# Optimization experiments

Hardware: AMD Instinct MI355X
Metric: run time of the kernel (lower is better)

The kernel has to match this reference:

```python
import jax, jax.numpy as jnp
import numpy as np

N_HEADS = 8


def setup_inputs() -> dict:
    key = jax.random.key(0)
    ks = jax.random.split(key, 6)
    B, U, Lx, Ly = 16, 512, 1024, 1024
    x = jax.random.normal(ks[0], (B, U, Lx), dtype=jnp.float32)
    y = jax.random.normal(ks[1], (B, U, Ly), dtype=jnp.float32)
    xy_mask = jax.random.randint(ks[2], (B, Lx, Ly), 0, 2).astype(jnp.bool_)
    wq = jax.random.normal(ks[3], (U, U), dtype=jnp.float32) * (1.0 / np.sqrt(U))
    wk = jax.random.normal(ks[4], (U, U), dtype=jnp.float32) * (1.0 / np.sqrt(U))
    wo = jax.random.normal(ks[5], (U, U), dtype=jnp.float32) * (1.0 / np.sqrt(U))
    return {"x": x, "y": y, "xy_mask": xy_mask, "wq": wq, "wk": wk, "wo": wo}


def reference(x, y, xy_mask, wq, wk, wo):
    # x: (B, U, Lx), y: (B, U, Ly), xy_mask: (B, Lx, Ly)
    B, U, Lx = x.shape
    Ly = y.shape[2]
    H = N_HEADS
    d = U // H
    scale = 1.0 / (d ** 0.5)

    # 1x1 conv (bias=False) == channel-mixing matmul; weight layout (out, in)
    Q = jnp.einsum('ou,bul->bol', wq, x)   # (B, U, Lx)
    K = jnp.einsum('ou,bul->bol', wk, y)   # (B, U, Ly)

    # split channels into heads (head-major channel order, matching torch.split)
    Qh = Q.reshape(B, H, d, Lx)
    Kh = K.reshape(B, H, d, Ly)

    # ReLU-scored attention with mask (no softmax)
    A = jnp.einsum('bhdx,bhdy->bhxy', Qh, Kh)           # (B, H, Lx, Ly)
    A = jnp.maximum(A, 0.0) * scale
    A = jnp.where(xy_mask[:, None, :, :], A, 0.0)

    C = jnp.einsum('bhxy,bhdy->bhdx', A, Kh).reshape(B, U, Lx)

    # per-row element-count normalization (rows with zero count use 1)
    n_el = jnp.maximum(jnp.sum(xy_mask, axis=2), 1)     # (B, Lx)
    C = C / n_el[:, None, :].astype(x.dtype)

    E = 0.5 * (Q + C)
    return jnp.einsum('ou,bul->bol', wo, E)
```

## Files before the change

kernel.cpp:

```cpp
#include <hip/hip_runtime.h>
#include <stdint.h>
#include <stddef.h>

#define B_  16
#define U_  512
#define LX_ 1024
#define LY_ 1024
#define H_  8
#define D_  64

typedef unsigned short ushort_t;
typedef unsigned int   uint_t;
typedef __bf16 v8bf  __attribute__((ext_vector_type(8)));
typedef float  v16f  __attribute__((ext_vector_type(16)));

__device__ __forceinline__ ushort_t bf16u(float f) {
    uint_t u = __float_as_uint(f);
    uint_t r = (u + 0x7FFFu + ((u >> 16) & 1u)) >> 16;
    return (ushort_t)r;
}
__device__ __forceinline__ float bfu2f(ushort_t u) {
    return __uint_as_float(((uint_t)u) << 16);
}
__device__ __forceinline__ uint_t pkbf16(float f0, float f1) {
    uint_t u0 = __float_as_uint(f0), u1 = __float_as_uint(f1);
    u0 = u0 + 0x7FFFu + ((u0 >> 16) & 1u);
    u1 = u1 + 0x7FFFu + ((u1 >> 16) & 1u);
    return __builtin_amdgcn_perm(u1, u0, 0x07060302u);
}
__device__ __forceinline__ void gload16(const void* g, void* l) {
    auto gp = (const __attribute__((address_space(1))) uint32_t*)(uintptr_t)g;
    auto lp = (__attribute__((address_space(3))) uint32_t*)(uintptr_t)l;
    __builtin_amdgcn_global_load_lds(gp, lp, 16, 0, 0);
}

__global__ __launch_bounds__(256) void prep_kernel(const float* __restrict__ X,
                                                   const float* __restrict__ Y,
                                                   const void* __restrict__ mask,
                                                   const float* __restrict__ wq,
                                                   const float* __restrict__ wk,
                                                   const float* __restrict__ wo,
                                                   ushort_t* __restrict__ XT,
                                                   ushort_t* __restrict__ YT,
                                                   ushort_t* __restrict__ wqb,
                                                   ushort_t* __restrict__ wkb,
                                                   ushort_t* __restrict__ wob,
                                                   float* __restrict__ nel,
                                                   uint_t* __restrict__ mb) {
    __shared__ uint_t Tp[64 * 33];
    const int tid = threadIdx.x;
    const int bid = blockIdx.x;

    if (bid < 4096) {
        const int l0 = (bid & 15) * 64;
        const int u0 = ((bid >> 4) & 7) * 64;
        const int z  = bid >> 7;
        const int b  = z & 15;
        const int sel = z >> 4;
        const float* S = sel ? Y : X;
        ushort_t*  Dst = sel ? YT : XT;
        #pragma unroll
        for (int e = 0; e < 4; ++e) {
            int ci = e * 256 + tid;
            int r = ci >> 4, c4 = (ci & 15) * 4;
            float4 v = *(const float4*)&S[((size_t)(b * U_ + u0 + r) << 10) + l0 + c4];
            Tp[r * 33 + (c4 >> 1)]     = pkbf16(v.x, v.y);
            Tp[r * 33 + (c4 >> 1) + 1] = pkbf16(v.z, v.w);
        }
        __syncthreads();
        #pragma unroll
        for (int e = 0; e < 2; ++e) {
            int ci = e * 256 + tid;
            int lr = ci >> 3, cc = ci & 7;
            int l2 = lr >> 1;
            uint_t sel8 = (lr & 1) ? 0x07060302u : 0x05040100u;
            uint_t wv[4];
            #pragma unroll
            for (int i = 0; i < 4; ++i) {
                uint_t A  = Tp[(cc * 8 + 2 * i) * 33 + l2];
                uint_t Bv = Tp[(cc * 8 + 2 * i + 1) * 33 + l2];
                wv[i] = __builtin_amdgcn_perm(Bv, A, sel8);
            }
            *(uint4*)&Dst[((size_t)((b << 10) + l0 + lr)) * U_ + u0 + cc * 8] = *(uint4*)wv;
        }
    } else if (bid < 8192) {
        const int lane = tid & 63;
        const uint4* m4 = (const uint4*)mask;
        uint4 dw = m4[lane];
        bool all4 = (dw.x <= 1u) && (dw.y <= 1u) && (dw.z <= 1u) && (dw.w <= 1u);
        const int isInt = (__popcll(__ballot(all4)) >= 32) ? 1 : 0;

        int row  = (bid - 4096) * 4 + (tid >> 6);
        const uint8_t* m8  = (const uint8_t*)mask + (size_t)row * LY_;
        const int*     m32 = (const int*)mask + (size_t)row * LY_;
        int cnt = 0;
        if (isInt) {
            #pragma unroll 4
            for (int yg = 0; yg < LY_ / 64; ++yg) {
                unsigned long long bal = __ballot(m32[yg * 64 + lane] != 0);
                if (lane == 0) {
                    mb[(size_t)row * 32 + yg * 2]     = (uint_t)bal;
                    mb[(size_t)row * 32 + yg * 2 + 1] = (uint_t)(bal >> 32);
                    cnt += __popcll(bal);
                }
            }
        } else {
            #pragma unroll 4
            for (int yg = 0; yg < LY_ / 64; ++yg) {
                unsigned long long bal = __ballot(m8[yg * 64 + lane] != 0);
                if (lane == 0) {
                    mb[(size_t)row * 32 + yg * 2]     = (uint_t)bal;
                    mb[(size_t)row * 32 + yg * 2 + 1] = (uint_t)(bal >> 32);
                    cnt += __popcll(bal);
                }
            }
        }
        if (lane == 0) nel[row] = (float)(cnt > 0 ? cnt : 1);
    } else {
        int cb = bid - 8192;
        int selw = cb >> 8;
        const float* sw = selw == 0 ? wq : (selw == 1 ? wk : wo);
        ushort_t*    dw = selw == 0 ? wqb : (selw == 1 ? wkb : wob);
        int i = ((cb & 255) * 256 + tid) * 4;
        float4 v = *(const float4*)&sw[i];
        ushort4 p;
        p.x = bf16u(v.x); p.y = bf16u(v.y); p.z = bf16u(v.z); p.w = bf16u(v.w);
        *(ushort4*)&dw[i] = p;
    }
}

__global__ __launch_bounds__(256) void gemm_qk(const ushort_t* __restrict__ xT,
                                               const ushort_t* __restrict__ wqb,
                                               const ushort_t* __restrict__ wkb,
                                               const ushort_t* __restrict__ yT,
                                               ushort_t* __restrict__ QT,
                                               ushort_t* __restrict__ Ka,
                                               ushort_t* __restrict__ Kb) {
    __shared__ __align__(16) ushort_t As[128 * 64];
    __shared__ __align__(16) ushort_t Bs[128 * 64];
    const int tid = threadIdx.x;
    const int id  = blockIdx.x;
    const int isK = id >> 9;
    const int lid = id & 511;
    const int b   = lid >> 5;
    int m0, n0, ldOut;
    const ushort_t *Ab, *Bb;
    ushort_t* Ob;
    if (!isK) {
        n0 = (lid & 3) * 128; m0 = ((lid >> 2) & 7) * 128;
        Ab = xT + (size_t)b * (LX_ * U_); Bb = wqb;
        Ob = QT + (size_t)b * (LX_ * U_); ldOut = U_;
    } else {
        n0 = (lid & 7) * 128; m0 = ((lid >> 3) & 3) * 128;
        Ab = wkb; Bb = yT + (size_t)b * (LY_ * U_);
        Ob = Ka + (size_t)b * (U_ * LY_); ldOut = LY_;
    }

    const int w = tid >> 6, lane = tid & 63, lo = lane & 31, hi = lane >> 5;
    const int wm = (w >> 1) * 64, wn = (w & 1) * 64;

    v16f acc00, acc01, acc10, acc11;
    #pragma unroll
    for (int i = 0; i < 16; ++i) { acc00[i] = 0.f; acc01[i] = 0.f; acc10[i] = 0.f; acc11[i] = 0.f; }

    for (int kk = 0; kk < 8; ++kk) {
        const int k0 = kk * 64;
        #pragma unroll
        for (int e = 0; e < 4; ++e) {
            int ci = e * 256 + tid;
            int r = ci >> 3, c = ci & 7;
            int g = (c ^ (r & 7)) << 3;
            gload16(&Ab[(size_t)(m0 + r) * U_ + k0 + g], &As[ci * 8]);
            gload16(&Bb[(size_t)(n0 + r) * U_ + k0 + g], &Bs[ci * 8]);
        }
        __syncthreads();
        #pragma unroll
        for (int ks = 0; ks < 4; ++ks) {
            int ch = ks * 2 + hi;
            int rA0 = wm + lo, rA1 = wm + 32 + lo;
            int rB0 = wn + lo, rB1 = wn + 32 + lo;
            v8bf a0 = *(v8bf*)&As[rA0 * 64 + ((ch ^ (rA0 & 7)) << 3)];
            v8bf a1 = *(v8bf*)&As[rA1 * 64 + ((ch ^ (rA1 & 7)) << 3)];
            v8bf b0 = *(v8bf*)&Bs[rB0 * 64 + ((ch ^ (rB0 & 7)) << 3)];
            v8bf b1 = *(v8bf*)&Bs[rB1 * 64 + ((ch ^ (rB1 & 7)) << 3)];
            acc00 = __builtin_amdgcn_mfma_f32_32x32x16_bf16(a0, b0, acc00, 0, 0, 0);
            acc01 = __builtin_amdgcn_mfma_f32_32x32x16_bf16(a0, b1, acc01, 0, 0, 0);
            acc10 = __builtin_amdgcn_mfma_f32_32x32x16_bf16(a1, b0, acc10, 0, 0, 0);
            acc11 = __builtin_amdgcn_mfma_f32_32x32x16_bf16(a1, b1, acc11, 0, 0, 0);
        }
        __syncthreads();
    }

    #pragma unroll
    for (int mi = 0; mi < 2; ++mi) {
        #pragma unroll
        for (int nj = 0; nj < 2; ++nj) {
            v16f c = mi ? (nj ? acc11 : acc10) : (nj ? acc01 : acc00);
            int n = n0 + wn + nj * 32 + lo;
            int mbase = m0 + wm + mi * 32;
            ushort_t us[16];
            #pragma unroll
            for (int r = 0; r < 16; ++r) {
                int m = mbase + (r & 3) + 8 * (r >> 2) + 4 * hi;
                ushort_t v = bf16u(c[r]);
                us[r] = v;
                Ob[(size_t)m * ldOut + n] = v;
            }
            if (isK) {
                int head = mbase >> 6;
                int db   = (mbase & 63) + 4 * hi;
                ushort_t* kbrow = Kb + (((size_t)(b * H_ + head) << 10) + n) * D_ + db;
                #pragma unroll
                for (int q = 0; q < 4; ++q) {
                    uint2 pk2;
                    pk2.x = (uint_t)us[q * 4 + 0] | ((uint_t)us[q * 4 + 1] << 16);
                    pk2.y = (uint_t)us[q * 4 + 2] | ((uint_t)us[q * 4 + 3] << 16);
                    *(uint2*)&kbrow[q * 8] = pk2;
                }
            }
        }
    }
}

template <int OUTF32>
__global__ __launch_bounds__(256) void gemm_mfma(const ushort_t* __restrict__ A, size_t aStr,
                                                 const ushort_t* __restrict__ Bm, size_t bStr,
                                                 void* __restrict__ Out, size_t oStr, int ldOut) {
    const int n0 = blockIdx.x * 128;
    const int m0 = blockIdx.y * 128;
    const int b  = blockIdx.z;
    __shared__ __align__(16) ushort_t As[128 * 64];
    __shared__ __align__(16) ushort_t Bs[128 * 64];
    const int tid = threadIdx.x;
    const ushort_t* Ab = A + aStr * b;
    const ushort_t* Bb = Bm + bStr * b;

    const int w = tid >> 6, lane = tid & 63, lo = lane & 31, hi = lane >> 5;
    const int wm = (w >> 1) * 64, wn = (w & 1) * 64;

    v16f acc00, acc01, acc10, acc11;
    #pragma unroll
    for (int i = 0; i < 16; ++i) { acc00[i] = 0.f; acc01[i] = 0.f; acc10[i] = 0.f; acc11[i] = 0.f; }

    for (int kk = 0; kk < 8; ++kk) {
        const int k0 = kk * 64;
        #pragma unroll
        for (int e = 0; e < 4; ++e) {
            int ci = e * 256 + tid;
            int r = ci >> 3, c = ci & 7;
            int g = (c ^ (r & 7)) << 3;
            gload16(&Ab[(size_t)(m0 + r) * U_ + k0 + g], &As[ci * 8]);
            gload16(&Bb[(size_t)(n0 + r) * U_ + k0 + g], &Bs[ci * 8]);
        }
        __syncthreads();
        #pragma unroll
        for (int ks = 0; ks < 4; ++ks) {
            int ch = ks * 2 + hi;
            int rA0 = wm + lo, rA1 = wm + 32 + lo;
            int rB0 = wn + lo, rB1 = wn + 32 + lo;
            v8bf a0 = *(v8bf*)&As[rA0 * 64 + ((ch ^ (rA0 & 7)) << 3)];
            v8bf a1 = *(v8bf*)&As[rA1 * 64 + ((ch ^ (rA1 & 7)) << 3)];
            v8bf b0 = *(v8bf*)&Bs[rB0 * 64 + ((ch ^ (rB0 & 7)) << 3)];
            v8bf b1 = *(v8bf*)&Bs[rB1 * 64 + ((ch ^ (rB1 & 7)) << 3)];
            acc00 = __builtin_amdgcn_mfma_f32_32x32x16_bf16(a0, b0, acc00, 0, 0, 0);
            acc01 = __builtin_amdgcn_mfma_f32_32x32x16_bf16(a0, b1, acc01, 0, 0, 0);
            acc10 = __builtin_amdgcn_mfma_f32_32x32x16_bf16(a1, b0, acc10, 0, 0, 0);
            acc11 = __builtin_amdgcn_mfma_f32_32x32x16_bf16(a1, b1, acc11, 0, 0, 0);
        }
        __syncthreads();
    }

    #pragma unroll
    for (int mi = 0; mi < 2; ++mi) {
        #pragma unroll
        for (int nj = 0; nj < 2; ++nj) {
            v16f c = mi ? (nj ? acc11 : acc10) : (nj ? acc01 : acc00);
            int n = n0 + wn + nj * 32 + lo;
            #pragma unroll
            for (int r = 0; r < 16; ++r) {
                int m = m0 + wm + mi * 32 + (r & 3) + 8 * (r >> 2) + 4 * hi;
                size_t addr = oStr * b + (size_t)m * ldOut + n;
                if (OUTF32) ((float*)Out)[addr] = c[r];
                else        ((ushort_t*)Out)[addr] = bf16u(c[r]);
            }
        }
    }
}

typedef uint_t v2u __attribute__((ext_vector_type(2)));

__device__ __forceinline__ void conv_sblock(const v16f& s, uint_t wbh, v8bf* fr) {
    uint_t pk[8];
    #pragma unroll
    for (int i = 0; i < 8; ++i) {
        float f0 = fmaxf(s[2 * i + 0], 0.f);
        float f1 = fmaxf(s[2 * i + 1], 0.f);
        uint_t r;
        asm("v_cvt_pk_bf16_f32 %0, %1, %2" : "=v"(r) : "v"(f0), "v"(f1));
        pk[i] = r;
    }
    #pragma unroll
    for (int t = 0; t < 2; ++t) {
        auto ra = __builtin_amdgcn_permlane32_swap(pk[4 * t + 0], pk[4 * t + 2], false, false);
        auto rb = __builtin_amdgcn_permlane32_swap(pk[4 * t + 1], pk[4 * t + 3], false, false);
        uint_t w0 = ra[0];
        uint_t w1 = rb[0];
        uint_t w2 = ra[1];
        uint_t w3 = rb[1];
        uint_t u0 = wbh >> (t * 16 + 0);
        uint_t u1 = wbh >> (t * 16 + 2);
        uint_t u2 = wbh >> (t * 16 + 4);
        uint_t u3 = wbh >> (t * 16 + 6);
        w0 &= ((u0 & 1u) * 0xFFFFu) | ((u0 & 2u) * 0x7FFF8000u);
        w1 &= ((u1 & 1u) * 0xFFFFu) | ((u1 & 2u) * 0x7FFF8000u);
        w2 &= ((u2 & 1u) * 0xFFFFu) | ((u2 & 2u) * 0x7FFF8000u);
        w3 &= ((u3 & 1u) * 0xFFFFu) | ((u3 & 2u) * 0x7FFF8000u);
        union { uint_t u[4]; v8bf b; } cv;
        cv.u[0] = w0; cv.u[1] = w1; cv.u[2] = w2; cv.u[3] = w3;
        fr[t] = cv.b;
    }
}

__global__ __launch_bounds__(256, 4) void attn_mfma(const ushort_t* __restrict__ QTg,
                                                    const ushort_t* __restrict__ Ka_g,
                                                    const ushort_t* __restrict__ Kb_g,
                                                    const uint_t* __restrict__ mbits,
                                                    const float* __restrict__ nel,
                                                    ushort_t* __restrict__ ETg) {
    const int tid = threadIdx.x;
    const int id  = blockIdx.x;
    const int bh  = id & 127;
    const int x0g = (id >> 7) * 128;
    const int b = bh >> 3, h = bh & 7;

    __shared__ __align__(16) ushort_t SM[4 * 4096];

    const int w    = tid >> 6;
    const int lane = tid & 63;
    const int lo   = lane & 31;
    const int hi   = lane >> 5;
    const int xq   = w * 32;

    const ushort_t* KaBase = Ka_g + ((size_t)(b * U_ + h * D_)) * LY_;
    const ushort_t* KbBase = Kb_g + ((size_t)(b * H_ + h)) * LY_ * D_;
    const int bx = b * LX_ + x0g;
    const int xg = bx + xq + lo;

    #pragma unroll
    for (int e = 0; e < 2; ++e) {
        int ci = e * 256 + tid;
        int r = ci >> 3, c = ci & 7;
        int g8 = (c ^ (r & 7)) << 3;
        gload16(&KbBase[(size_t)r * D_ + g8], &SM[ci * 8]);
        gload16(&KaBase[(size_t)r * LY_ + g8], &SM[8192 + ci * 8]);
    }

    v8bf qf[4];
    {
        const ushort_t* q0 = QTg + (size_t)xg * U_ + h * D_;
        #pragma unroll
        for (int kt = 0; kt < 4; ++kt) qf[kt] = *(const v8bf*)&q0[(kt * 2 + hi) * 8];
    }

    v16f acc0, acc1;
    #pragma unroll
    for (int i = 0; i < 16; ++i) { acc0[i] = 0.f; acc1[i] = 0.f; }

    __syncthreads();

    #pragma unroll 2
    for (int tt = 0; tt < 16; ++tt) {
        ushort_t* KBc = SM + (tt & 1) * 4096;
        ushort_t* KAc = SM + 8192 + (tt & 1) * 4096;

        if (tt < 15) {
            ushort_t* KBn = SM + ((tt + 1) & 1) * 4096;
            ushort_t* KAn = SM + 8192 + ((tt + 1) & 1) * 4096;
            const int yn = tt * 64 + 64;
            #pragma unroll
            for (int e = 0; e < 2; ++e) {
                int ci = e * 256 + tid;
                int r = ci >> 3, c = ci & 7;
                int g8 = (c ^ (r & 7)) << 3;
                gload16(&KbBase[(size_t)(yn + r) * D_ + g8], &KBn[ci * 8]);
                gload16(&KaBase[(size_t)r * LY_ + yn + g8], &KAn[ci * 8]);
            }
        }
        v2u wb = *(const v2u*)&mbits[(size_t)xg * 32 + tt * 2];

        v8bf fr0[2], fr1[2];
        {
            v16f s;
            #pragma unroll
            for (int i = 0; i < 16; ++i) s[i] = 0.f;
            #pragma unroll
            for (int kt = 0; kt < 4; ++kt) {
                int ch = kt * 2 + hi;
                v8bf a = *(v8bf*)&KBc[lo * 64 + ((ch ^ (lo & 7)) << 3)];
                s = __builtin_amdgcn_mfma_f32_32x32x16_bf16(a, qf[kt], s, 0, 0, 0);
            }
            conv_sblock(s, wb[0] >> (hi * 8), fr0);
        }
        {
            v16f s;
            #pragma unroll
            for (int i = 0; i < 16; ++i) s[i] = 0.f;
            #pragma unroll
            for (int kt = 0; kt < 4; ++kt) {
                int ch = kt * 2 + hi;
                v8bf a = *(v8bf*)&KBc[(32 + lo) * 64 + ((ch ^ ((32 + lo) & 7)) << 3)];
                s = __builtin_amdgcn_mfma_f32_32x32x16_bf16(a, qf[kt], s, 0, 0, 0);
            }
            conv_sblock(s, wb[1] >> (hi * 8), fr1);
        }

        #pragma unroll
        for (int kt = 0; kt < 4; ++kt) {
            int ch = kt * 2 + hi;
            v8bf frk = (kt < 2) ? fr0[kt] : fr1[kt - 2];
            v8bf a0 = *(v8bf*)&KAc[lo * 64 + ((ch ^ (lo & 7)) << 3)];
            v8bf a1 = *(v8bf*)&KAc[(32 + lo) * 64 + ((ch ^ ((32 + lo) & 7)) << 3)];
            acc0 = __builtin_amdgcn_mfma_f32_32x32x16_bf16(a0, frk, acc0, 0, 0, 0);
            acc1 = __builtin_amdgcn_mfma_f32_32x32x16_bf16(a1, frk, acc1, 0, 0, 0);
        }
        __syncthreads();
    }

    {
        ushort_t* Et = SM;
        const int xl = xq + lo;
        float invn = 0.0625f / nel[xg];
        const ushort_t* qg = QTg + (size_t)xg * U_ + h * D_ + 4 * hi;
        #pragma unroll
        for (int half = 0; half < 2; ++half) {
            const v16f& c = half ? acc1 : acc0;
            #pragma unroll
            for (int q = 0; q < 4; ++q) {
                int d0 = half * 32 + q * 8 + 4 * hi;
                ushort_t q4[4];
                *(uint2*)q4 = *(const uint2*)&qg[half * 32 + q * 8];
                ushort_t e4[4];
                e4[0] = bf16u(0.5f * bfu2f(q4[0]) + c[q * 4 + 0] * invn);
                e4[1] = bf16u(0.5f * bfu2f(q4[1]) + c[q * 4 + 1] * invn);
                e4[2] = bf16u(0.5f * bfu2f(q4[2]) + c[q * 4 + 2] * invn);
                e4[3] = bf16u(0.5f * bfu2f(q4[3]) + c[q * 4 + 3] * invn);
                int base = xl * 64 + ((((d0 >> 3) ^ (xl & 7)) << 3) | (4 * hi));
                *(uint2*)&Et[base] = *(uint2*)e4;
            }
        }
    }
    __syncthreads();
    #pragma unroll
    for (int e = 0; e < 4; ++e) {
        int idx = e * 256 + tid;
        int row = idx >> 3, cc = idx & 7;
        uint4 v = *(const uint4*)&SM[row * 64 + ((cc ^ (row & 7)) << 3)];
        *(uint4*)&ETg[((size_t)(bx + row)) * U_ + h * D_ + cc * 8] = v;
    }
}

extern "C" void kernel_launch(void* const* d_in, const int* in_sizes, int n_in,
                              void* d_out, int out_size, void* d_ws, size_t ws_size,
                              hipStream_t stream) {
    const float* x    = (const float*)d_in[0];
    const float* y    = (const float*)d_in[1];
    const void*  mask = d_in[2];
    const float* wq   = (const float*)d_in[3];
    const float* wk   = (const float*)d_in[4];
    const float* wo   = (const float*)d_in[5];

    char* wsb = (char*)d_ws;
    ushort_t* xT    = (ushort_t*)(wsb);
    ushort_t* yT    = (ushort_t*)(wsb + 16777216);
    ushort_t* Ka    = (ushort_t*)(wsb + 33554432);
    ushort_t* wqb   = (ushort_t*)(wsb + 50331648);
    ushort_t* wkb   = (ushort_t*)(wsb + 50855936);
    ushort_t* wob   = (ushort_t*)(wsb + 51380224);
    uint_t*   mbits = (uint_t*)(wsb + 51904512);
    float*    nel   = (float*)(wsb + 54001664);
    ushort_t* ET    = xT;
    ushort_t* QT    = (ushort_t*)d_out;
    ushort_t* Kb    = (ushort_t*)d_out + (size_t)B_ * LX_ * U_;

    prep_kernel<<<8960, 256, 0, stream>>>(x, y, mask, wq, wk, wo,
                                          xT, yT, wqb, wkb, wob, nel, mbits);
    gemm_qk<<<1024, 256, 0, stream>>>(xT, wqb, wkb, yT, QT, Ka, Kb);
    attn_mfma<<<1024, 256, 0, stream>>>(QT, Ka, Kb, mbits, nel, ET);
    gemm_mfma<1><<<dim3(8, 4, B_), 256, 0, stream>>>(
        wob, 0, ET, (size_t)LX_ * U_, d_out, (size_t)U_ * LX_, LX_);
}
```

Measured before the change: 279.3 us.

## Split prep kernel; use async LDS loads for transpose and vectorized mask packing

```diff
diff --git a/kernel.cpp b/kernel.cpp
--- a/kernel.cpp
+++ b/kernel.cpp
@@ -34,90 +34,97 @@
     __builtin_amdgcn_global_load_lds(gp, lp, 16, 0, 0);
 }
 
-__global__ __launch_bounds__(256) void prep_kernel(const float* __restrict__ X,
-                                                   const float* __restrict__ Y,
-                                                   const void* __restrict__ mask,
+__global__ __launch_bounds__(256) void castT_kernel(const float* __restrict__ X,
+                                                    const float* __restrict__ Y,
+                                                    ushort_t* __restrict__ XT,
+                                                    ushort_t* __restrict__ YT) {
+    __shared__ __align__(16) float Tf[64 * 64];
+    const int tid = threadIdx.x;
+    const int bid = blockIdx.x;
+    const int l0 = (bid & 15) * 64;
+    const int u0 = ((bid >> 4) & 7) * 64;
+    const int z  = bid >> 7;
+    const int b  = z & 15;
+    const int sel = z >> 4;
+    const float* S = sel ? Y : X;
+    ushort_t*  Dst = sel ? YT : XT;
+
+    #pragma unroll
+    for (int e = 0; e < 4; ++e) {
+        int ci = e * 256 + tid;
+        int r = ci >> 4, c = ci & 15;
+        int g = (c ^ ((r >> 3) & 7)) << 2;
+        gload16(&S[((size_t)(b * U_ + u0 + r) << 10) + l0 + g], &Tf[ci * 4]);
+    }
+    __syncthreads();
+    #pragma unroll
+    for (int e = 0; e < 2; ++e) {
+        int idx = e * 256 + tid;
+        int lr = idx >> 3, uo = idx & 7;
+        float f[8];
+        #pragma unroll
+        for (int k = 0; k < 8; ++k) {
+            int u = uo * 8 + k;
+            int c = (lr >> 2) ^ uo;
+            f[k] = Tf[u * 64 + c * 4 + (lr & 3)];
+        }
+        uint_t wv[4];
+        #pragma unroll
+        for (int j = 0; j < 4; ++j) wv[j] = pkbf16(f[2 * j], f[2 * j + 1]);
+        *(uint4*)&Dst[((size_t)((b << 10) + l0 + lr)) * U_ + u0 + uo * 8] = *(uint4*)wv;
+    }
+}
+
+__global__ __launch_bounds__(256) void nelw_kernel(const void* __restrict__ mask,
                                                    const float* __restrict__ wq,
                                                    const float* __restrict__ wk,
                                                    const float* __restrict__ wo,
-                                                   ushort_t* __restrict__ XT,
-                                                   ushort_t* __restrict__ YT,
                                                    ushort_t* __restrict__ wqb,
                                                    ushort_t* __restrict__ wkb,
                                                    ushort_t* __restrict__ wob,
                                                    float* __restrict__ nel,
                                                    uint_t* __restrict__ mb) {
-    __shared__ uint_t Tp[64 * 33];
     const int tid = threadIdx.x;
     const int bid = blockIdx.x;
-
     if (bid < 4096) {
-        const int l0 = (bid & 15) * 64;
-        const int u0 = ((bid >> 4) & 7) * 64;
-        const int z  = bid >> 7;
-        const int b  = z & 15;
-        const int sel = z >> 4;
-        const float* S = sel ? Y : X;
-        ushort_t*  Dst = sel ? YT : XT;
-        #pragma unroll
-        for (int e = 0; e < 4; ++e) {
-            int ci = e * 256 + tid;
-            int r = ci >> 4, c4 = (ci & 15) * 4;
-            float4 v = *(const float4*)&S[((size_t)(b * U_ + u0 + r) << 10) + l0 + c4];
-            Tp[r * 33 + (c4 >> 1)]     = pkbf16(v.x, v.y);
-            Tp[r * 33 + (c4 >> 1) + 1] = pkbf16(v.z, v.w);
-        }
-        __syncthreads();
-        #pragma unroll
-        for (int e = 0; e < 2; ++e) {
-            int ci = e * 256 + tid;
-            int lr = ci >> 3, cc = ci & 7;
-            int l2 = lr >> 1;
-            uint_t sel8 = (lr & 1) ? 0x07060302u : 0x05040100u;
-            uint_t wv[4];
-            #pragma unroll
-            for (int i = 0; i < 4; ++i) {
-                uint_t A  = Tp[(cc * 8 + 2 * i) * 33 + l2];
-                uint_t Bv = Tp[(cc * 8 + 2 * i + 1) * 33 + l2];
-                wv[i] = __builtin_amdgcn_perm(Bv, A, sel8);
-            }
-            *(uint4*)&Dst[((size_t)((b << 10) + l0 + lr)) * U_ + u0 + cc * 8] = *(uint4*)wv;
-        }
-    } else if (bid < 8192) {
         const int lane = tid & 63;
-        const uint4* m4 = (const uint4*)mask;
-        uint4 dw = m4[lane];
+        uint4 dw = ((const uint4*)mask)[lane];
         bool all4 = (dw.x <= 1u) && (dw.y <= 1u) && (dw.z <= 1u) && (dw.w <= 1u);
         const int isInt = (__popcll(__ballot(all4)) >= 32) ? 1 : 0;
 
-        int row  = (bid - 4096) * 4 + (tid >> 6);
-        const uint8_t* m8  = (const uint8_t*)mask + (size_t)row * LY_;
-        const int*     m32 = (const int*)mask + (size_t)row * LY_;
-        int cnt = 0;
+        const int row = bid * 4 + (tid >> 6);
+        uint_t m16 = 0;
         if (isInt) {
-            #pragma unroll 4
-            for (int yg = 0; yg < LY_ / 64; ++yg) {
-                unsigned long long bal = __ballot(m32[yg * 64 + lane] != 0);
-                if (lane == 0) {
-                    mb[(size_t)row * 32 + yg * 2]     = (uint_t)bal;
-                    mb[(size_t)row * 32 + yg * 2 + 1] = (uint_t)(bal >> 32);
-                    cnt += __popcll(bal);
-                }
+            const uint4* mr = (const uint4*)((const int*)mask + (size_t)row * LY_);
+            #pragma unroll
+            for (int i = 0; i < 4; ++i) {
+                uint4 v = mr[lane * 4 + i];
+                uint_t m4 = (v.x != 0 ? 1u : 0u) | (v.y != 0 ? 2u : 0u)
+                          | (v.z != 0 ? 4u : 0u) | (v.w != 0 ? 8u : 0u);
+                m16 |= m4 << (4 * i);
             }
         } else {
-            #pragma unroll 4
-            for (int yg = 0; yg < LY_ / 64; ++yg) {
-                unsigned long long bal = __ballot(m8[yg * 64 + lane] != 0);
-                if (lane == 0) {
-                    mb[(size_t)row * 32 + yg * 2]     = (uint_t)bal;
-                    mb[(size_t)row * 32 + yg * 2 + 1] = (uint_t)(bal >> 32);
-                    cnt += __popcll(bal);
-                }
-            }
-        }
+            const uint4* mr = (const uint4*)((const uint8_t*)mask + (size_t)row * LY_);
+            uint4 v = mr[lane];
+            uint_t d[4] = {v.x, v.y, v.z, v.w};
+            #pragma unroll
+            for (int i = 0; i < 4; ++i) {
+                uint_t u = d[i];
+                uint_t nz = (u | ((u & 0x7F7F7F7Fu) + 0x7F7F7F7Fu)) & 0x80808080u;
+                uint_t m4 = ((nz >> 7) & 1u) | ((nz >> 14) & 2u)
+                          | ((nz >> 21) & 4u) | ((nz >> 28) & 8u);
+                m16 |= m4 << (4 * i);
+            }
+        }
+        uint_t other = (uint_t)__shfl_xor((int)m16, 1);
+        if ((lane & 1) == 0)
+            mb[(size_t)row * 32 + (lane >> 1)] = m16 | (other << 16);
+        int cnt = __popc(m16);
+        #pragma unroll
+        for (int o = 1; o < 64; o <<= 1) cnt += __shfl_xor(cnt, o);
         if (lane == 0) nel[row] = (float)(cnt > 0 ? cnt : 1);
     } else {
-        int cb = bid - 8192;
+        int cb = bid - 4096;
         int selw = cb >> 8;
         const float* sw = selw == 0 ? wq : (selw == 1 ? wk : wo);
         ushort_t*    dw = selw == 0 ? wqb : (selw == 1 ? wkb : wob);
@@ -482,8 +489,8 @@
     ushort_t* QT    = (ushort_t*)d_out;
     ushort_t* Kb    = (ushort_t*)d_out + (size_t)B_ * LX_ * U_;
 
-    prep_kernel<<<8960, 256, 0, stream>>>(x, y, mask, wq, wk, wo,
-                                          xT, yT, wqb, wkb, wob, nel, mbits);
+    castT_kernel<<<4096, 256, 0, stream>>>(x, y, xT, yT);
+    nelw_kernel<<<4864, 256, 0, stream>>>(mask, wq, wk, wo, wqb, wkb, wob, nel, mbits);
     gemm_qk<<<1024, 256, 0, stream>>>(xT, wqb, wkb, yT, QT, Ka, Kb);
     attn_mfma<<<1024, 256, 0, stream>>>(QT, Ka, Kb, mbits, nel, ET);
     gemm_mfma<1><<<dim3(8, 4, B_), 256, 0, stream>>>(
```

Result: faster. 264.0 us (-5.4%).
